# Kernel tuning notes

Hardware: AMD Instinct MI355X
Metric: run time of the kernel (lower is better)

Reference implementation:

```python
import jax, jax.numpy as jnp
import numpy as np

N = 100000
E = 800000
DIMS = [128, 128, 128, 256, 256]  # layer in/out widths
NUM_CLASSES = 4


def _xavier(key, shape, gain):
    fan_in, fan_out = shape[0], shape[1]
    bound = gain * np.sqrt(6.0 / (fan_in + fan_out))
    return jax.random.uniform(key, shape, jnp.float32, -bound, bound)


def setup_inputs() -> dict:
    key = jax.random.key(0)
    ks = jax.random.split(key, 8)
    gain = np.sqrt(2.0)  # calculate_gain('relu')
    inp = {
        "x": jax.random.normal(ks[0], (N, DIMS[0]), jnp.float32),
        "src": jax.random.randint(ks[1], (E,), 0, N, jnp.int32),
        "dst": jax.random.randint(ks[2], (E,), 0, N, jnp.int32),
    }
    for i in range(4):
        inp[f"W{i}"] = _xavier(ks[3 + i], (DIMS[i], DIMS[i + 1]), gain)
        inp[f"b{i}"] = jnp.zeros((DIMS[i + 1],), jnp.float32)
    inp["Wc"] = _xavier(ks[7], (DIMS[4], NUM_CLASSES), gain)
    inp["bc"] = jnp.zeros((NUM_CLASSES,), jnp.float32)
    return inp


def _graph_conv(x, W, b, src, dst, norm_src, norm_dst):
    # DGL GraphConv, norm='both': scale by out-deg^-1/2, W, SpMM (sum over
    # edges src->dst), scale by in-deg^-1/2, +bias, ReLU. (A(XW)=(AX)W so
    # weight-order branch in DGL is math-equivalent.)
    h = (x * norm_src) @ W                      # [N, out]
    agg = jax.ops.segment_sum(h[src], dst, num_segments=x.shape[0])
    return jax.nn.relu(agg * norm_dst + b)


def reference(x, src, dst, W0, b0, W1, b1, W2, b2, W3, b3, Wc, bc):
    ones = jnp.ones((src.shape[0],), jnp.float32)
    deg_out = jnp.clip(jax.ops.segment_sum(ones, src, num_segments=N), 1.0)
    deg_in = jnp.clip(jax.ops.segment_sum(ones, dst, num_segments=N), 1.0)
    norm_src = (deg_out ** -0.5)[:, None]
    norm_dst = (deg_in ** -0.5)[:, None]
    h = x
    for W, b in ((W0, b0), (W1, b1), (W2, b2), (W3, b3)):
        h = _graph_conv(h, W, b, src, dst, norm_src, norm_dst)
        # dropout(p=0.5) is identity in eval mode
    return h @ Wc + bc
```

## Files before the change

### kernel.cpp

```cpp
#include <hip/hip_runtime.h>
#include <cstdint>
#include <cstddef>

#define NN 100000
#define NEDGE 800000
#define NBUCK 196
#define RNG 512
#define CAP 5120

typedef __attribute__((ext_vector_type(8))) short short8v;
typedef __attribute__((ext_vector_type(16))) float float16v;

__device__ inline ushort f2bf(float f) {
    uint32_t u = __float_as_uint(f);
    u += 0x7fff + ((u >> 16) & 1);
    return (ushort)(u >> 16);
}
__device__ inline float bf2f(ushort h) { return __uint_as_float(((uint32_t)h) << 16); }

__device__ inline void gload16(const void* g, void* lds) {
    __builtin_amdgcn_global_load_lds(
        (const __attribute__((address_space(1))) void*)g,
        (__attribute__((address_space(3))) void*)lds, 16, 0, 0);
}


__global__ void initCur(int* __restrict__ dstCur, int* __restrict__ srcCur) {
    int i = threadIdx.x;
    if (i < NBUCK) { dstCur[i] = i * CAP; srcCur[i] = i * CAP; }
}

__global__ __launch_bounds__(256) void partition_kernel(
        const int* __restrict__ src, const int* __restrict__ dst,
        int* __restrict__ dstCur, int* __restrict__ srcCur,
        int2* __restrict__ pairBuck, int* __restrict__ srcBuck, int E) {
    __shared__ int cd[NBUCK], bd[NBUCK], cs[NBUCK], bs[NBUCK];
    const int CH = (E + gridDim.x - 1) / gridDim.x;
    const int lo = blockIdx.x * CH;
    const int hi = min(lo + CH, E);
    for (int i = threadIdx.x; i < NBUCK; i += 256) { cd[i] = 0; cs[i] = 0; }
    __syncthreads();
    for (int i = lo + threadIdx.x; i < hi; i += 256) {
        atomicAdd(&cd[dst[i] >> 9], 1);
        atomicAdd(&cs[src[i] >> 9], 1);
    }
    __syncthreads();
    for (int i = threadIdx.x; i < NBUCK; i += 256) {
        bd[i] = cd[i] ? atomicAdd(&dstCur[i], cd[i]) : 0;
        bs[i] = cs[i] ? atomicAdd(&srcCur[i], cs[i]) : 0;
        cd[i] = 0; cs[i] = 0;
    }
    __syncthreads();
    for (int i = lo + threadIdx.x; i < hi; i += 256) {
        int s = src[i], d = dst[i];
        int slot = atomicAdd(&cd[d >> 9], 1);
        pairBuck[bd[d >> 9] + slot] = make_int2(s, d);
        int slot2 = atomicAdd(&cs[s >> 9], 1);
        srcBuck[bs[s >> 9] + slot2] = s;
    }
}

__global__ __launch_bounds__(256) void srcHistConv(
        const int* __restrict__ srcBuck, const int* __restrict__ srcCur,
        const float* __restrict__ x, float* __restrict__ ns,
        ushort* __restrict__ actB, int n) {
    __shared__ int h[RNG];
    __shared__ float sns[RNG];
    const int k = blockIdx.x;
    for (int i = threadIdx.x; i < RNG; i += 256) h[i] = 0;
    __syncthreads();
    const int lo = k * CAP, hi = srcCur[k];
    for (int i = lo + threadIdx.x; i < hi; i += 256)
        atomicAdd(&h[srcBuck[i] & (RNG - 1)], 1);
    __syncthreads();
    for (int i = threadIdx.x; i < RNG; i += 256) {
        float v = 1.0f / sqrtf((float)max(h[i], 1));
        sns[i] = v;
        int idx = k * RNG + i;
        if (idx < n) ns[idx] = v;
    }
    __syncthreads();
    const int base = k * RNG;
    for (int i = threadIdx.x; i < RNG * 32; i += 256) {
        int nl = i >> 5;
        int node = base + nl;
        if (node < n) {
            int f0 = (i & 31) * 4;
            float sc = sns[nl];
            float4 v = *reinterpret_cast<const float4*>(x + (size_t)node * 128 + f0);
            ushort4 hh;
            hh.x = f2bf(v.x * sc);
            hh.y = f2bf(v.y * sc);
            hh.z = f2bf(v.z * sc);
            hh.w = f2bf(v.w * sc);
            *reinterpret_cast<ushort4*>(actB + (size_t)node * 128 + f0) = hh;
        }
    }
}

__global__ __launch_bounds__(256) void dstBuild(const int2* __restrict__ pairBuck,
                                                const int* __restrict__ dstCur,
                                                float* __restrict__ nd, int2* __restrict__ rowse,
                                                int* __restrict__ permSrc, int n) {
    __shared__ int h[RNG];
    __shared__ int tsum[256];
    const int k = blockIdx.x;
    const int t = threadIdx.x;
    for (int i = t; i < RNG; i += 256) h[i] = 0;
    __syncthreads();
    const int lo = k * CAP, hi = dstCur[k];
    for (int i = lo + t; i < hi; i += 256)
        atomicAdd(&h[pairBuck[i].y & (RNG - 1)], 1);
    __syncthreads();
    int a0 = h[2 * t], a1 = h[2 * t + 1];
    tsum[t] = a0 + a1;
    __syncthreads();
    for (int off = 1; off < 256; off <<= 1) {
        int v = (t >= off) ? tsum[t - off] : 0;
        __syncthreads();
        tsum[t] += v;
        __syncthreads();
    }
    const int pre = lo + (t > 0 ? tsum[t - 1] : 0);
    const int r0 = pre, r1 = pre + a0;
    const int idx0 = k * RNG + 2 * t;
    if (idx0 < n)     { rowse[idx0]     = make_int2(r0, r1);      nd[idx0]     = 1.0f / sqrtf((float)max(a0, 1)); }
    if (idx0 + 1 < n) { rowse[idx0 + 1] = make_int2(r1, r1 + a1); nd[idx0 + 1] = 1.0f / sqrtf((float)max(a1, 1)); }
    h[2 * t] = r0;
    h[2 * t + 1] = r1;
    __syncthreads();
    for (int i = lo + t; i < hi; i += 256) {
        int2 p = pairBuck[i];
        int pos = atomicAdd(&h[p.y & (RNG - 1)], 1);
        permSrc[pos] = p.x;
    }
}


__global__ void convw_all(const float* __restrict__ W0, const float* __restrict__ W1,
                          const float* __restrict__ W2, const float* __restrict__ W3,
                          ushort* __restrict__ Wt) {
    int idx = blockIdx.x * blockDim.x + threadIdx.x;
    if (idx >= 131072) return;
    const float* W; int K, logD, base;
    if (idx < 16384)      { W = W0; K = 128; logD = 7; base = 0; }
    else if (idx < 32768) { W = W1; K = 128; logD = 7; base = 16384; }
    else if (idx < 65536) { W = W2; K = 128; logD = 8; base = 32768; }
    else                  { W = W3; K = 256; logD = 8; base = 65536; }
    int loc = idx - base;
    int k = loc >> logD, d = loc & ((1 << logD) - 1);
    Wt[base + d * K + k] = f2bf(W[loc]);
}


__device__ inline void accum8(float* a, uint4 v) {
    a[0] += __uint_as_float(v.x << 16);
    a[1] += __uint_as_float(v.x & 0xffff0000u);
    a[2] += __uint_as_float(v.y << 16);
    a[3] += __uint_as_float(v.y & 0xffff0000u);
    a[4] += __uint_as_float(v.z << 16);
    a[5] += __uint_as_float(v.z & 0xffff0000u);
    a[6] += __uint_as_float(v.w << 16);
    a[7] += __uint_as_float(v.w & 0xffff0000u);
}

template<int D>
__global__ __launch_bounds__(256) void agg_kernel(
        const ushort* __restrict__ act, const int2* __restrict__ rowse,
        const int* __restrict__ permSrc, const float* __restrict__ nd,
        ushort* __restrict__ Rb, int n) {
    int node = blockIdx.x * 4 + (threadIdx.x >> 6);
    if (node >= n) return;
    int lane = threadIdx.x & 63;
    constexpr int GROUPS = (D == 256) ? 2 : 4;
    constexpr int GL = 64 / GROUPS;
    const int g  = lane / GL;
    const int gl = lane % GL;
    const int f0 = gl * 8;
    float a[8] = {0.f,0.f,0.f,0.f,0.f,0.f,0.f,0.f};
    int2 se = rowse[node];
    int r0 = se.x, r1 = se.y;

    int e = r0 + g;
    for (; e + 3 * GROUPS < r1; e += 4 * GROUPS) {
        int s0 = permSrc[e];
        int s1 = permSrc[e + GROUPS];
        int s2 = permSrc[e + 2 * GROUPS];
        int s3 = permSrc[e + 3 * GROUPS];
        uint4 v0 = *reinterpret_cast<const uint4*>(act + (size_t)s0 * D + f0);
        uint4 v1 = *reinterpret_cast<const uint4*>(act + (size_t)s1 * D + f0);
        uint4 v2 = *reinterpret_cast<const uint4*>(act + (size_t)s2 * D + f0);
        uint4 v3 = *reinterpret_cast<const uint4*>(act + (size_t)s3 * D + f0);
        accum8(a, v0); accum8(a, v1); accum8(a, v2); accum8(a, v3);
    }
    for (; e < r1; e += GROUPS) {
        int s = permSrc[e];
        accum8(a, *reinterpret_cast<const uint4*>(act + (size_t)s * D + f0));
    }

    #pragma unroll
    for (int j = 0; j < 8; j++) {
        if constexpr (GROUPS == 4) a[j] += __shfl_xor(a[j], 16);
        a[j] += __shfl_xor(a[j], 32);
    }

    if (g == 0) {
        float sc = nd[node];
        union { ushort u[8]; uint4 v; } H;
        #pragma unroll
        for (int j = 0; j < 8; j++) H.u[j] = f2bf(a[j] * sc);
        *reinterpret_cast<uint4*>(Rb + (size_t)node * D + f0) = H.v;
    }
}


__global__ __launch_bounds__(256) void gemm_mfma(
        const ushort* __restrict__ A, const ushort* __restrict__ B,
        const float* __restrict__ bias, const float* __restrict__ post,
        ushort* __restrict__ Cb, int n, int K, int Dout, int logCB, int nrowp) {
    __shared__ __align__(16) ushort sA[128][64];
    __shared__ __align__(16) ushort sB[64][64];
    const int tid = threadIdx.x;
    const int lane = tid & 63;
    const int wid = tid >> 6;
    const int l31 = lane & 31;
    const int kg = lane >> 5;

    const int bid = blockIdx.x;
    const int xcd = bid & 7;
    const int t = bid >> 3;
    const int cb2 = t & ((1 << logCB) - 1);
    const int rp = (t >> logCB) * 8 + xcd;
    if (rp >= nrowp) return;
    const int row0 = rp * 128;
    const int col0 = cb2 * 64;

    const ushort* gA[4];
    char* lA[4];
    #pragma unroll
    for (int i = 0; i < 4; i++) {
        int slot = i * 256 + wid * 64 + lane;
        int r = slot >> 3, ch = slot & 7;
        int gch = ch ^ (r & 7);
        int row = row0 + r; if (row >= n) row = n - 1;
        gA[i] = A + (size_t)row * K + gch * 8;
        lA[i] = (char*)&sA[0][0] + (size_t)(i * 256 + wid * 64) * 16;
    }
    const ushort* gB[2];
    char* lB[2];
    #pragma unroll
    for (int i = 0; i < 2; i++) {
        int slot = i * 256 + wid * 64 + lane;
        int r = slot >> 3, ch = slot & 7;
        int gch = ch ^ (r & 7);
        gB[i] = B + (size_t)(col0 + r) * K + gch * 8;
        lB[i] = (char*)&sB[0][0] + (size_t)(i * 256 + wid * 64) * 16;
    }

    float16v acc0 = {0.f,0.f,0.f,0.f,0.f,0.f,0.f,0.f,0.f,0.f,0.f,0.f,0.f,0.f,0.f,0.f};
    float16v acc1 = {0.f,0.f,0.f,0.f,0.f,0.f,0.f,0.f,0.f,0.f,0.f,0.f,0.f,0.f,0.f,0.f};

    for (int k0 = 0; k0 < K; k0 += 64) {
        #pragma unroll
        for (int i = 0; i < 4; i++) gload16(gA[i] + k0, lA[i]);
        #pragma unroll
        for (int i = 0; i < 2; i++) gload16(gB[i] + k0, lB[i]);
        __syncthreads();

        #pragma unroll
        for (int ks = 0; ks < 4; ks++) {
            const int gw = ks * 2 + kg;
            const int rA = wid * 32 + l31;
            const int rB0 = l31, rB1 = 32 + l31;
            short8v a = *reinterpret_cast<const short8v*>(&sA[rA][(gw ^ (rA & 7)) * 8]);
            short8v b0 = *reinterpret_cast<const short8v*>(&sB[rB0][(gw ^ (rB0 & 7)) * 8]);
            short8v b1 = *reinterpret_cast<const short8v*>(&sB[rB1][(gw ^ (rB1 & 7)) * 8]);
            acc0 = __builtin_amdgcn_mfma_f32_32x32x16_bf16(a, b0, acc0, 0, 0, 0);
            acc1 = __builtin_amdgcn_mfma_f32_32x32x16_bf16(a, b1, acc1, 0, 0, 0);
        }
        __syncthreads();
    }

    const int rbase = row0 + wid * 32;
    #pragma unroll
    for (int cb = 0; cb < 2; cb++) {
        const int colg = col0 + cb * 32 + l31;
        const float bcol = bias[colg];
        const float16v& acc = cb ? acc1 : acc0;
        #pragma unroll
        for (int r = 0; r < 16; r++) {
            int rowg = rbase + (r & 3) + 8 * (r >> 2) + 4 * kg;
            if (rowg < n) {
                float v = fmaxf(acc[r] + bcol, 0.0f);
                if (post) v *= post[rowg];
                Cb[(size_t)rowg * Dout + colg] = f2bf(v);
            }
        }
    }
}


__global__ __launch_bounds__(256) void classifier_kernel(
        const ushort* __restrict__ h, const float* __restrict__ Wc,
        const float* __restrict__ bc, float* __restrict__ out, int n) {
    __shared__ float Ws[256 * 4];
    int tid = threadIdx.x;
    for (int i = tid; i < 1024; i += 256) Ws[i] = Wc[i];
    __syncthreads();
    int node = blockIdx.x * 64 + (tid >> 2);
    int c = tid & 3;
    if (node < n) {
        float sum = bc[c];
        const ushort* hr = h + (size_t)node * 256;
        #pragma unroll
        for (int k0 = 0; k0 < 256; k0 += 8) {
            uint4 pk = *reinterpret_cast<const uint4*>(hr + k0);
            sum = fmaf(bf2f((ushort)(pk.x & 0xffff)), Ws[(k0 + 0) * 4 + c], sum);
            sum = fmaf(bf2f((ushort)(pk.x >> 16)),    Ws[(k0 + 1) * 4 + c], sum);
            sum = fmaf(bf2f((ushort)(pk.y & 0xffff)), Ws[(k0 + 2) * 4 + c], sum);
            sum = fmaf(bf2f((ushort)(pk.y >> 16)),    Ws[(k0 + 3) * 4 + c], sum);
            sum = fmaf(bf2f((ushort)(pk.z & 0xffff)), Ws[(k0 + 4) * 4 + c], sum);
            sum = fmaf(bf2f((ushort)(pk.z >> 16)),    Ws[(k0 + 5) * 4 + c], sum);
            sum = fmaf(bf2f((ushort)(pk.w & 0xffff)), Ws[(k0 + 6) * 4 + c], sum);
            sum = fmaf(bf2f((ushort)(pk.w >> 16)),    Ws[(k0 + 7) * 4 + c], sum);
        }
        out[(size_t)node * 4 + c] = sum;
    }
}


extern "C" void kernel_launch(void* const* d_in, const int* in_sizes, int n_in,
                              void* d_out, int out_size, void* d_ws, size_t ws_size,
                              hipStream_t stream) {
    const float* x   = (const float*)d_in[0];
    const int*   src = (const int*)d_in[1];
    const int*   dst = (const int*)d_in[2];
    const float* W0 = (const float*)d_in[3];
    const float* b0 = (const float*)d_in[4];
    const float* W1 = (const float*)d_in[5];
    const float* b1 = (const float*)d_in[6];
    const float* W2 = (const float*)d_in[7];
    const float* b2 = (const float*)d_in[8];
    const float* W3 = (const float*)d_in[9];
    const float* b3 = (const float*)d_in[10];
    const float* Wc = (const float*)d_in[11];
    const float* bc = (const float*)d_in[12];
    const float* b[4] = {b0, b1, b2, b3};
    float* out = (float*)d_out;

    ushort* actB = (ushort*)d_ws;
    ushort* Rb   = actB + (size_t)NN * 256;
    float*  ns   = (float*)(Rb + (size_t)NN * 256);
    float*  nd   = ns + NN;
    ushort* Wt   = (ushort*)(nd + NN);
    int2*   rowse   = (int2*)(Wt + 131072);
    int*    permSrc = (int*)(rowse + NN);
    int*    dstCur  = permSrc + NBUCK * CAP;
    int*    srcCur  = dstCur + NBUCK;
    int2*   pairBuck = (int2*)Rb;
    int*    srcBuck  = (int*)(pairBuck + NBUCK * CAP);
    (void)in_sizes; (void)n_in; (void)out_size; (void)ws_size;

    initCur<<<1, 256, 0, stream>>>(dstCur, srcCur);
    partition_kernel<<<256, 256, 0, stream>>>(src, dst, dstCur, srcCur, pairBuck, srcBuck, NEDGE);
    convw_all<<<512, 256, 0, stream>>>(W0, W1, W2, W3, Wt);
    srcHistConv<<<NBUCK, 256, 0, stream>>>(srcBuck, srcCur, x, ns, actB, NN);
    dstBuild<<<NBUCK, 256, 0, stream>>>(pairBuck, dstCur, nd, rowse, permSrc, NN);

    const int dims[5] = {128, 128, 128, 256, 256};
    const int woff[4] = {0, 16384, 32768, 65536};
    const int nrowp = (NN + 127) / 128;
    const int nrowp8 = ((nrowp + 7) / 8) * 8;

    for (int l = 0; l < 4; l++) {
        int K = dims[l], Dout = dims[l + 1];
        int logCB = (Dout == 128) ? 1 : 2;
        int CB = Dout / 64;

        int ablocks = (NN + 3) / 4;
        if (K == 128)
            agg_kernel<128><<<ablocks, 256, 0, stream>>>(actB, rowse, permSrc, nd, Rb, NN);
        else
            agg_kernel<256><<<ablocks, 256, 0, stream>>>(actB, rowse, permSrc, nd, Rb, NN);

        const float* post = (l < 3) ? ns : nullptr;
        gemm_mfma<<<nrowp8 * CB, 256, 0, stream>>>(Rb, Wt + woff[l], b[l], post,
                                                   actB, NN, K, Dout, logCB, nrowp);
    }

    classifier_kernel<<<(NN + 63) / 64, 256, 0, stream>>>(actB, Wc, bc, out, NN);
}
```

Before: 399.6 us.

## Compute full output width per GEMM block and unroll aggregation tail loop

Result: slower. 570.3 us (+42.7%).

```diff
diff --git a/kernel.cpp b/kernel.cpp
--- a/kernel.cpp
+++ b/kernel.cpp
@@ -193,7 +193,14 @@
         uint4 v3 = *reinterpret_cast<const uint4*>(act + (size_t)s3 * D + f0);
         accum8(a, v0); accum8(a, v1); accum8(a, v2); accum8(a, v3);
     }
-    for (; e < r1; e += GROUPS) {
+    for (; e + GROUPS < r1; e += 2 * GROUPS) {
+        int s0 = permSrc[e];
+        int s1 = permSrc[e + GROUPS];
+        uint4 v0 = *reinterpret_cast<const uint4*>(act + (size_t)s0 * D + f0);
+        uint4 v1 = *reinterpret_cast<const uint4*>(act + (size_t)s1 * D + f0);
+        accum8(a, v0); accum8(a, v1);
+    }
+    if (e < r1) {
         int s = permSrc[e];
         accum8(a, *reinterpret_cast<const uint4*>(act + (size_t)s * D + f0));
     }
@@ -214,12 +221,14 @@
 }
 
 
-__global__ __launch_bounds__(256) void gemm_mfma(
+template<int CB>
+__global__ __launch_bounds__(256) void gemm_full(
         const ushort* __restrict__ A, const ushort* __restrict__ B,
         const float* __restrict__ bias, const float* __restrict__ post,
-        ushort* __restrict__ Cb, int n, int K, int Dout, int logCB, int nrowp) {
+        ushort* __restrict__ Cb, int n, int K, int nrowp) {
+    constexpr int Dout = CB * 64;
     __shared__ __align__(16) ushort sA[128][64];
-    __shared__ __align__(16) ushort sB[64][64];
+    __shared__ __align__(16) ushort sB[CB][64][64];
     const int tid = threadIdx.x;
     const int lane = tid & 63;
     const int wid = tid >> 6;
@@ -227,13 +236,9 @@
     const int kg = lane >> 5;
 
     const int bid = blockIdx.x;
-    const int xcd = bid & 7;
-    const int t = bid >> 3;
-    const int cb2 = t & ((1 << logCB) - 1);
-    const int rp = (t >> logCB) * 8 + xcd;
+    const int rp = (bid >> 3) * 8 + (bid & 7);
     if (rp >= nrowp) return;
     const int row0 = rp * 128;
-    const int col0 = cb2 * 64;
 
     const ushort* gA[4];
     char* lA[4];
@@ -246,54 +251,67 @@
         gA[i] = A + (size_t)row * K + gch * 8;
         lA[i] = (char*)&sA[0][0] + (size_t)(i * 256 + wid * 64) * 16;
     }
-    const ushort* gB[2];
-    char* lB[2];
+    const ushort* gB[CB][2];
+    char* lB[CB][2];
     #pragma unroll
-    for (int i = 0; i < 2; i++) {
-        int slot = i * 256 + wid * 64 + lane;
-        int r = slot >> 3, ch = slot & 7;
-        int gch = ch ^ (r & 7);
-        gB[i] = B + (size_t)(col0 + r) * K + gch * 8;
-        lB[i] = (char*)&sB[0][0] + (size_t)(i * 256 + wid * 64) * 16;
-    }
-
-    float16v acc0 = {0.f,0.f,0.f,0.f,0.f,0.f,0.f,0.f,0.f,0.f,0.f,0.f,0.f,0.f,0.f,0.f};
-    float16v acc1 = {0.f,0.f,0.f,0.f,0.f,0.f,0.f,0.f,0.f,0.f,0.f,0.f,0.f,0.f,0.f,0.f};
+    for (int cb = 0; cb < CB; cb++) {
+        #pragma unroll
+        for (int i = 0; i < 2; i++) {
+            int slot = i * 256 + wid * 64 + lane;
+            int r = slot >> 3, ch = slot & 7;
+            int gch = ch ^ (r & 7);
+            gB[cb][i] = B + (size_t)(cb * 64 + r) * K + gch * 8;
+            lB[cb][i] = (char*)&sB[cb][0][0] + (size_t)(i * 256 + wid * 64) * 16;
+        }
+    }
+
+    float16v acc[CB][2];
+    #pragma unroll
+    for (int cb = 0; cb < CB; cb++)
+        #pragma unroll
+        for (int h = 0; h < 2; h++)
+            acc[cb][h] = (float16v){0.f,0.f,0.f,0.f,0.f,0.f,0.f,0.f,0.f,0.f,0.f,0.f,0.f,0.f,0.f,0.f};
 
     for (int k0 = 0; k0 < K; k0 += 64) {
         #pragma unroll
         for (int i = 0; i < 4; i++) gload16(gA[i] + k0, lA[i]);
         #pragma unroll
-        for (int i = 0; i < 2; i++) gload16(gB[i] + k0, lB[i]);
+        for (int cb = 0; cb < CB; cb++)
+            #pragma unroll
+            for (int i = 0; i < 2; i++) gload16(gB[cb][i] + k0, lB[cb][i]);
         __syncthreads();
 
         #pragma unroll
         for (int ks = 0; ks < 4; ks++) {
             const int gw = ks * 2 + kg;
             const int rA = wid * 32 + l31;
-            const int rB0 = l31, rB1 = 32 + l31;
             short8v a = *reinterpret_cast<const short8v*>(&sA[rA][(gw ^ (rA & 7)) * 8]);
-            short8v b0 = *reinterpret_cast<const short8v*>(&sB[rB0][(gw ^ (rB0 & 7)) * 8]);
-            short8v b1 = *reinterpret_cast<const short8v*>(&sB[rB1][(gw ^ (rB1 & 7)) * 8]);
-            acc0 = __builtin_amdgcn_mfma_f32_32x32x16_bf16(a, b0, acc0, 0, 0, 0);
-            acc1 = __builtin_amdgcn_mfma_f32_32x32x16_bf16(a, b1, acc1, 0, 0, 0);
+            #pragma unroll
+            for (int cb = 0; cb < CB; cb++) {
+                short8v b0 = *reinterpret_cast<const short8v*>(&sB[cb][l31][(gw ^ (l31 & 7)) * 8]);
+                short8v b1 = *reinterpret_cast<const short8v*>(&sB[cb][32 + l31][(gw ^ (l31 & 7)) * 8]);
+                acc[cb][0] = __builtin_amdgcn_mfma_f32_32x32x16_bf16(a, b0, acc[cb][0], 0, 0, 0);
+                acc[cb][1] = __builtin_amdgcn_mfma_f32_32x32x16_bf16(a, b1, acc[cb][1], 0, 0, 0);
+            }
         }
         __syncthreads();
     }
 
     const int rbase = row0 + wid * 32;
     #pragma unroll
-    for (int cb = 0; cb < 2; cb++) {
-        const int colg = col0 + cb * 32 + l31;
-        const float bcol = bias[colg];
-        const float16v& acc = cb ? acc1 : acc0;
-        #pragma unroll
-        for (int r = 0; r < 16; r++) {
-            int rowg = rbase + (r & 3) + 8 * (r >> 2) + 4 * kg;
-            if (rowg < n) {
-                float v = fmaxf(acc[r] + bcol, 0.0f);
-                if (post) v *= post[rowg];
-                Cb[(size_t)rowg * Dout + colg] = f2bf(v);
+    for (int cb = 0; cb < CB; cb++) {
+        #pragma unroll
+        for (int h = 0; h < 2; h++) {
+            const int colg = cb * 64 + h * 32 + l31;
+            const float bcol = bias[colg];
+            #pragma unroll
+            for (int r = 0; r < 16; r++) {
+                int rowg = rbase + (r & 3) + 8 * (r >> 2) + 4 * kg;
+                if (rowg < n) {
+                    float v = fmaxf(acc[cb][h][r] + bcol, 0.0f);
+                    if (post) v *= post[rowg];
+                    Cb[(size_t)rowg * Dout + colg] = f2bf(v);
+                }
             }
         }
     }
@@ -374,8 +392,6 @@
 
     for (int l = 0; l < 4; l++) {
         int K = dims[l], Dout = dims[l + 1];
-        int logCB = (Dout == 128) ? 1 : 2;
-        int CB = Dout / 64;
 
         int ablocks = (NN + 3) / 4;
         if (K == 128)
@@ -384,8 +400,10 @@
             agg_kernel<256><<<ablocks, 256, 0, stream>>>(actB, rowse, permSrc, nd, Rb, NN);
 
         const float* post = (l < 3) ? ns : nullptr;
-        gemm_mfma<<<nrowp8 * CB, 256, 0, stream>>>(Rb, Wt + woff[l], b[l], post,
-                                                   actB, NN, K, Dout, logCB, nrowp);
+        if (Dout == 128)
+            gemm_full<2><<<nrowp8, 256, 0, stream>>>(Rb, Wt + woff[l], b[l], post, actB, NN, K, nrowp);
+        else
+            gemm_full<4><<<nrowp8, 256, 0, stream>>>(Rb, Wt + woff[l], b[l], post, actB, NN, K, nrowp);
     }
 
     classifier_kernel<<<(NN + 63) / 64, 256, 0, stream>>>(actB, Wc, bc, out, NN);
```
